# Kernel optimization log

Hardware: AMD Instinct MI355X
Metric: run time of the kernel (lower is better)

## Reference

```python
import jax, jax.numpy as jnp
import numpy as np

B, D, K, L, C = 1024, 512, 255, 256, 80  # batch, feat, internal nodes, leaves, classes
DEPTH = 8  # complete binary tree: 2^8 = 256 leaves


def _build_res_path():
    # res_path[l, k] = 1 if internal node k is on leaf l's path and leaf goes left,
    # -1 if it goes right, 0 if node k not on the path (matches build_tree_squeeze).
    rp = np.zeros((L, K), dtype=np.int32)
    for leaf in range(L):
        node = 0
        for d in range(DEPTH):
            bit = (leaf >> (DEPTH - 1 - d)) & 1  # 0 -> left, 1 -> right
            rp[leaf, node] = 1 if bit == 0 else -1
            node = 2 * node + 1 + bit
    return jnp.asarray(rp)


def setup_inputs() -> dict:
    key = jax.random.key(0)
    k1, k2, k3, k4 = jax.random.split(key, 4)
    x = jax.random.normal(k1, (B, D), dtype=jnp.float32)
    node_embeddings = jax.random.normal(k2, (K, D), dtype=jnp.float32)
    leaf_W = jax.random.normal(k3, (L * C, D), dtype=jnp.float32) * (1.0 / np.sqrt(D))
    leaf_b = jax.random.normal(k4, (L * C,), dtype=jnp.float32) * 0.01
    res_path = _build_res_path()
    return {"x": x, "node_embeddings": node_embeddings, "leaf_W": leaf_W,
            "leaf_b": leaf_b, "res_path": res_path}


def reference(x, node_embeddings, leaf_W, leaf_b, res_path):
    # L2-normalize node embeddings, cosine-sim routing probabilities
    ne = node_embeddings / jnp.linalg.norm(node_embeddings, axis=-1, keepdims=True)
    node_sim = jax.nn.sigmoid(jnp.einsum('bc,kc->bk', x, ne))  # [B, K]
    # leaf decision logits: Linear(D, L*C) reshaped to [B, L, C]
    leaf_dec = (jnp.einsum('bc,oc->bo', x, leaf_W) + leaf_b).reshape(x.shape[0], L, C)
    left_mask = (res_path == 1)[None]    # [1, L, K]
    right_mask = (res_path == -1)[None]  # [1, L, K]
    ns = node_sim[:, None, :]            # [B, 1, K]
    prob_left = jnp.prod(jnp.where(left_mask, ns, 1.0), axis=-1)        # [B, L]
    prob_right = jnp.prod(jnp.where(right_mask, 1.0 - ns, 1.0), axis=-1)  # [B, L]
    probs = (prob_left * prob_right)[..., None] * leaf_dec  # [B, L, C]
    return probs.sum(axis=1), node_sim
```

## Files before the change

kernel.cpp:

```cpp
#include <hip/hip_runtime.h>
#include <stdint.h>

#define B_  1024
#define D_  512
#define K_  255
#define L_  256
#define C_  80

typedef __attribute__((ext_vector_type(8))) short bf16x8;
typedef __attribute__((ext_vector_type(4))) float f32x4;

#define GLD(gsrc, ldst) \
  __builtin_amdgcn_global_load_lds((const __attribute__((address_space(1))) void*)(gsrc), \
                                   (__attribute__((address_space(3))) void*)(ldst), 16, 0, 0)

__device__ __forceinline__ short cvt_bf16(float f) {
    unsigned u = __float_as_uint(f);
    u += 0x7FFFu + ((u >> 16) & 1u);
    return (short)(u >> 16);
}

typedef __attribute__((ext_vector_type(8))) short short8;

__global__ void convert_kernel(const float* __restrict__ w, const float* __restrict__ x,
                               short* __restrict__ wb, short* __restrict__ xb) {
    size_t i0 = (size_t)blockIdx.x * blockDim.x + threadIdx.x;
    size_t stride = (size_t)gridDim.x * blockDim.x;
    for (size_t v = i0; v < 1310720u; v += stride) {
        float4 a = ((const float4*)w)[v * 2];
        float4 b = ((const float4*)w)[v * 2 + 1];
        short8 o;
        o[0] = cvt_bf16(a.x); o[1] = cvt_bf16(a.y); o[2] = cvt_bf16(a.z); o[3] = cvt_bf16(a.w);
        o[4] = cvt_bf16(b.x); o[5] = cvt_bf16(b.y); o[6] = cvt_bf16(b.z); o[7] = cvt_bf16(b.w);
        ((short8*)wb)[v] = o;
    }
    for (size_t v = i0; v < 65536u; v += stride) {
        float4 a = ((const float4*)x)[v * 2];
        float4 b = ((const float4*)x)[v * 2 + 1];
        short8 o;
        o[0] = cvt_bf16(a.x); o[1] = cvt_bf16(a.y); o[2] = cvt_bf16(a.z); o[3] = cvt_bf16(a.w);
        o[4] = cvt_bf16(b.x); o[5] = cvt_bf16(b.y); o[6] = cvt_bf16(b.z); o[7] = cvt_bf16(b.w);
        ((short8*)xb)[v] = o;
    }
}

__global__ __launch_bounds__(256) void node_kernel(const float* __restrict__ x,
                                                   const float* __restrict__ ne,
                                                   float* __restrict__ out1,
                                                   float* __restrict__ p_ws) {
    __shared__ __align__(16) float xs[4 * D_];
    __shared__ float ss[4 * K_];
    const int t = threadIdx.x;
    const int b0 = blockIdx.x * 4;

    const float4* xg = (const float4*)(x + (size_t)b0 * D_);
    ((float4*)xs)[t]       = xg[t];
    ((float4*)xs)[t + 256] = xg[t + 256];
    __syncthreads();

    if (t < K_) {
        const float4* nr = (const float4*)(ne + (size_t)t * D_);
        float acc0 = 0.f, acc1 = 0.f, acc2 = 0.f, acc3 = 0.f, nrm = 0.f;
        #pragma unroll 4
        for (int d4 = 0; d4 < D_ / 4; ++d4) {
            float4 nv = nr[d4];
            nrm += nv.x * nv.x + nv.y * nv.y + nv.z * nv.z + nv.w * nv.w;
            float4 x0 = ((const float4*)xs)[d4];
            float4 x1 = ((const float4*)xs)[128 + d4];
            float4 x2 = ((const float4*)xs)[256 + d4];
            float4 x3 = ((const float4*)xs)[384 + d4];
            acc0 += nv.x * x0.x + nv.y * x0.y + nv.z * x0.z + nv.w * x0.w;
            acc1 += nv.x * x1.x + nv.y * x1.y + nv.z * x1.z + nv.w * x1.w;
            acc2 += nv.x * x2.x + nv.y * x2.y + nv.z * x2.z + nv.w * x2.w;
            acc3 += nv.x * x3.x + nv.y * x3.y + nv.z * x3.z + nv.w * x3.w;
        }
        float inv = rsqrtf(nrm);
        float a[4] = {acc0, acc1, acc2, acc3};
        #pragma unroll
        for (int b = 0; b < 4; ++b) {
            float sig = 1.f / (1.f + __expf(-a[b] * inv));
            ss[b * K_ + t] = sig;
            out1[(size_t)(b0 + b) * K_ + t] = sig;
        }
    }
    __syncthreads();

    #pragma unroll
    for (int b = 0; b < 4; ++b) {
        float prob = 1.f;
        int node = 0;
        #pragma unroll
        for (int d = 0; d < 8; ++d) {
            int bit = (t >> (7 - d)) & 1;
            float s = ss[b * K_ + node];
            prob *= bit ? (1.f - s) : s;
            node = 2 * node + 1 + bit;
        }
        p_ws[(size_t)(b0 + b) * L_ + t] = prob;
    }
}

__global__ __launch_bounds__(256, 2) void gemm_kernel(const short* __restrict__ xb,
                                                      const short* __restrict__ wb,
                                                      const float* __restrict__ p,
                                                      const float* __restrict__ lb,
                                                      float* __restrict__ partial) {
    __shared__ __align__(16) short Ald[1024 * 8];
    __shared__ __align__(16) short Bld[640 * 8];
    __shared__ float p_ld[128];
    __shared__ float b_ld[80];

    const int tid  = threadIdx.x;
    const int lane = tid & 63;
    const int wave = tid >> 6;
    const int q    = lane >> 4;
    const int r    = lane & 15;
    const int wrow = wave * 32;
    const int mt   = blockIdx.x & 7;
    const int lc   = blockIdx.x >> 3;

    f32x4 outacc[2][5];
    #pragma unroll
    for (int mf = 0; mf < 2; ++mf)
        #pragma unroll
        for (int nf = 0; nf < 5; ++nf)
            outacc[mf][nf] = (f32x4){0.f, 0.f, 0.f, 0.f};

    const bf16x8* Av = (const bf16x8*)Ald;
    const bf16x8* Bv = (const bf16x8*)Bld;

    for (int li = 0; li < 4; ++li) {
        const int l = lc * 4 + li;
        f32x4 dec[2][5];
        #pragma unroll
        for (int mf = 0; mf < 2; ++mf)
            #pragma unroll
            for (int nf = 0; nf < 5; ++nf)
                dec[mf][nf] = (f32x4){0.f, 0.f, 0.f, 0.f};

        for (int kb = 0; kb < 8; ++kb) {
            __syncthreads();
            #pragma unroll
            for (int j = 0; j < 4; ++j) {
                int ph = j * 256 + tid;
                int rr = ph >> 3;
                int g  = (ph & 7) ^ (rr & 7);
                const short* src = xb + ((size_t)(mt * 128 + rr) * D_ + kb * 64 + g * 8);
                GLD(src, Ald + ph * 8);
            }
            #pragma unroll
            for (int j = 0; j < 2; ++j) {
                int ph = j * 256 + tid;
                int cc = ph >> 3;
                int g  = (ph & 7) ^ (cc & 7);
                const short* src = wb + ((size_t)(l * C_ + cc) * D_ + kb * 64 + g * 8);
                GLD(src, Bld + ph * 8);
            }
            if (tid < 128) {
                int ph = 512 + tid;
                int cc = ph >> 3;
                int g  = (ph & 7) ^ (cc & 7);
                const short* src = wb + ((size_t)(l * C_ + cc) * D_ + kb * 64 + g * 8);
                GLD(src, Bld + ph * 8);
            }
            if (kb == 0) {
                if (tid < 128) p_ld[tid] = p[(size_t)(mt * 128 + tid) * L_ + l];
                if (tid < 80)  b_ld[tid] = lb[l * C_ + tid];
            }
            __syncthreads();

            #pragma unroll
            for (int ks = 0; ks < 2; ++ks) {
                const int g = ks * 4 + q;
                bf16x8 af[2], bfr[5];
                #pragma unroll
                for (int mf = 0; mf < 2; ++mf) {
                    int rl = wrow + mf * 16 + r;
                    af[mf] = Av[rl * 8 + (g ^ (rl & 7))];
                }
                #pragma unroll
                for (int nf = 0; nf < 5; ++nf) {
                    int cl = nf * 16 + r;
                    bfr[nf] = Bv[cl * 8 + (g ^ (cl & 7))];
                }
                #pragma unroll
                for (int mf = 0; mf < 2; ++mf)
                    #pragma unroll
                    for (int nf = 0; nf < 5; ++nf)
                        dec[mf][nf] = __builtin_amdgcn_mfma_f32_16x16x32_bf16(
                            af[mf], bfr[nf], dec[mf][nf], 0, 0, 0);
            }
        }

        #pragma unroll
        for (int mf = 0; mf < 2; ++mf) {
            #pragma unroll
            for (int nf = 0; nf < 5; ++nf) {
                float bv = b_ld[nf * 16 + r];
                #pragma unroll
                for (int i = 0; i < 4; ++i) {
                    int row = wrow + mf * 16 + q * 4 + i;
                    outacc[mf][nf][i] += p_ld[row] * (dec[mf][nf][i] + bv);
                }
            }
        }
    }

    const size_t rbase = (size_t)lc * B_ + mt * 128;
    #pragma unroll
    for (int mf = 0; mf < 2; ++mf)
        #pragma unroll
        for (int nf = 0; nf < 5; ++nf)
            #pragma unroll
            for (int i = 0; i < 4; ++i) {
                int row = wrow + mf * 16 + q * 4 + i;
                int col = nf * 16 + r;
                partial[(rbase + row) * C_ + col] = outacc[mf][nf][i];
            }
}

__global__ void reduce_kernel(const float* __restrict__ partial, float* __restrict__ out0) {
    int idx = blockIdx.x * 256 + threadIdx.x;
    float s = 0.f;
    #pragma unroll 8
    for (int j = 0; j < 64; ++j)
        s += partial[(size_t)j * (B_ * C_) + idx];
    out0[idx] = s;
}

extern "C" void kernel_launch(void* const* d_in, const int* in_sizes, int n_in,
                              void* d_out, int out_size, void* d_ws, size_t ws_size,
                              hipStream_t stream) {
    const float* x  = (const float*)d_in[0];
    const float* ne = (const float*)d_in[1];
    const float* lW = (const float*)d_in[2];
    const float* lb = (const float*)d_in[3];

    float* out0 = (float*)d_out;
    float* out1 = out0 + (size_t)B_ * C_;

    char* ws = (char*)d_ws;
    float* p_ws    = (float*)ws;
    short* xb      = (short*)(ws + (1u << 20));
    short* wb      = (short*)(ws + (2u << 20));
    float* partial = (float*)(ws + (22u << 20));

    convert_kernel<<<2048, 256, 0, stream>>>(lW, x, wb, xb);
    node_kernel<<<B_ / 4, 256, 0, stream>>>(x, ne, out1, p_ws);
    gemm_kernel<<<512, 256, 0, stream>>>(xb, wb, p_ws, lb, partial);
    reduce_kernel<<<(B_ * C_) / 256, 256, 0, stream>>>(partial, out0);
}
```

Before: 154.8 us.

## Move node similarity to bf16 MFMA GEMM and restructure leaf GEMM tiling

Node embeddings are L2-normalized and converted to bf16 inside the convert kernel. The node-similarity dot products then run as a small MFMA GEMM in place of the scalar FP32 loop, and leaf probabilities are computed in a separate small kernel. The main leaf GEMM now gives each block two leaves (160 columns) over the full K with no outer leaf loop, uses 1024 blocks with a higher occupancy hint, and writes 128 partial slices, so the reduce kernel sums twice as many partials. This trades more partial-sum traffic and an extra launch for better MFMA use and parallelism, and node_sim now carries bf16 precision error.

New measurement: 143.1 us. -7.5%, faster.

```diff
diff --git a/kernel.cpp b/kernel.cpp
--- a/kernel.cpp
+++ b/kernel.cpp
@@ -9,6 +9,7 @@
 
 typedef __attribute__((ext_vector_type(8))) short bf16x8;
 typedef __attribute__((ext_vector_type(4))) float f32x4;
+typedef __attribute__((ext_vector_type(8))) short short8;
 
 #define GLD(gsrc, ldst) \
   __builtin_amdgcn_global_load_lds((const __attribute__((address_space(1))) void*)(gsrc), \
@@ -20,210 +21,227 @@
     return (short)(u >> 16);
 }
 
-typedef __attribute__((ext_vector_type(8))) short short8;
-
-__global__ void convert_kernel(const float* __restrict__ w, const float* __restrict__ x,
-                               short* __restrict__ wb, short* __restrict__ xb) {
-    size_t i0 = (size_t)blockIdx.x * blockDim.x + threadIdx.x;
-    size_t stride = (size_t)gridDim.x * blockDim.x;
-    for (size_t v = i0; v < 1310720u; v += stride) {
-        float4 a = ((const float4*)w)[v * 2];
-        float4 b = ((const float4*)w)[v * 2 + 1];
-        short8 o;
-        o[0] = cvt_bf16(a.x); o[1] = cvt_bf16(a.y); o[2] = cvt_bf16(a.z); o[3] = cvt_bf16(a.w);
-        o[4] = cvt_bf16(b.x); o[5] = cvt_bf16(b.y); o[6] = cvt_bf16(b.z); o[7] = cvt_bf16(b.w);
-        ((short8*)wb)[v] = o;
-    }
-    for (size_t v = i0; v < 65536u; v += stride) {
-        float4 a = ((const float4*)x)[v * 2];
-        float4 b = ((const float4*)x)[v * 2 + 1];
-        short8 o;
-        o[0] = cvt_bf16(a.x); o[1] = cvt_bf16(a.y); o[2] = cvt_bf16(a.z); o[3] = cvt_bf16(a.w);
-        o[4] = cvt_bf16(b.x); o[5] = cvt_bf16(b.y); o[6] = cvt_bf16(b.z); o[7] = cvt_bf16(b.w);
-        ((short8*)xb)[v] = o;
-    }
-}
-
-__global__ __launch_bounds__(256) void node_kernel(const float* __restrict__ x,
-                                                   const float* __restrict__ ne,
-                                                   float* __restrict__ out1,
-                                                   float* __restrict__ p_ws) {
-    __shared__ __align__(16) float xs[4 * D_];
-    __shared__ float ss[4 * K_];
-    const int t = threadIdx.x;
-    const int b0 = blockIdx.x * 4;
-
-    const float4* xg = (const float4*)(x + (size_t)b0 * D_);
-    ((float4*)xs)[t]       = xg[t];
-    ((float4*)xs)[t + 256] = xg[t + 256];
+__global__ __launch_bounds__(256) void convert_kernel(const float* __restrict__ w,
+                                                      const float* __restrict__ x,
+                                                      const float* __restrict__ ne,
+                                                      short* __restrict__ wb,
+                                                      short* __restrict__ xb,
+                                                      short* __restrict__ neb) {
+    __shared__ float red[256];
+    const int tid = threadIdx.x;
+    if (blockIdx.x < 2048) {
+        size_t i0 = (size_t)blockIdx.x * 256 + tid;
+        const size_t stride = 2048u * 256u;
+        for (size_t v = i0; v < 1310720u; v += stride) {
+            float4 a = ((const float4*)w)[v * 2];
+            float4 b = ((const float4*)w)[v * 2 + 1];
+            short8 o;
+            o[0] = cvt_bf16(a.x); o[1] = cvt_bf16(a.y); o[2] = cvt_bf16(a.z); o[3] = cvt_bf16(a.w);
+            o[4] = cvt_bf16(b.x); o[5] = cvt_bf16(b.y); o[6] = cvt_bf16(b.z); o[7] = cvt_bf16(b.w);
+            ((short8*)wb)[v] = o;
+        }
+        for (size_t v = i0; v < 65536u; v += stride) {
+            float4 a = ((const float4*)x)[v * 2];
+            float4 b = ((const float4*)x)[v * 2 + 1];
+            short8 o;
+            o[0] = cvt_bf16(a.x); o[1] = cvt_bf16(a.y); o[2] = cvt_bf16(a.z); o[3] = cvt_bf16(a.w);
+            o[4] = cvt_bf16(b.x); o[5] = cvt_bf16(b.y); o[6] = cvt_bf16(b.z); o[7] = cvt_bf16(b.w);
+            ((short8*)xb)[v] = o;
+        }
+    } else {
+        const int row = blockIdx.x - 2048;
+        if (row == 255) {
+            ((unsigned*)(neb + 255 * 512))[tid] = 0u;
+            return;
+        }
+        const float2* nr = (const float2*)(ne + (size_t)row * 512);
+        float2 a = nr[tid];
+        red[tid] = a.x * a.x + a.y * a.y;
+        __syncthreads();
+        #pragma unroll
+        for (int s = 128; s > 0; s >>= 1) {
+            if (tid < s) red[tid] += red[tid + s];
+            __syncthreads();
+        }
+        float inv = rsqrtf(red[0]);
+        unsigned lo = (unsigned short)cvt_bf16(a.x * inv);
+        unsigned hi = (unsigned short)cvt_bf16(a.y * inv);
+        ((unsigned*)(neb + (size_t)row * 512))[tid] = lo | (hi << 16);
+    }
+}
+
+__global__ __launch_bounds__(256) void simgemm_kernel(const short* __restrict__ xb,
+                                                      const short* __restrict__ neb,
+                                                      float* __restrict__ out1) {
+    __shared__ __align__(16) short Ald[512 * 8];
+    __shared__ __align__(16) short Bld[512 * 8];
+    const int tid = threadIdx.x;
+    const int lane = tid & 63, wave = tid >> 6;
+    const int q = lane >> 4, r = lane & 15;
+    const int mt = blockIdx.x >> 2;
+    const int nt = blockIdx.x & 3;
+
+    f32x4 acc[4];
+    #pragma unroll
+    for (int nf = 0; nf < 4; ++nf) acc[nf] = (f32x4){0.f, 0.f, 0.f, 0.f};
+
+    const bf16x8* Av = (const bf16x8*)Ald;
+    const bf16x8* Bv = (const bf16x8*)Bld;
+
+    for (int kb = 0; kb < 8; ++kb) {
+        __syncthreads();
+        #pragma unroll
+        for (int j = 0; j < 2; ++j) {
+            int ph = j * 256 + tid, rr = ph >> 3, g = (ph & 7) ^ (rr & 7);
+            GLD(xb + ((size_t)(mt * 64 + rr) * D_ + kb * 64 + g * 8), Ald + ph * 8);
+        }
+        #pragma unroll
+        for (int j = 0; j < 2; ++j) {
+            int ph = j * 256 + tid, cc = ph >> 3, g = (ph & 7) ^ (cc & 7);
+            GLD(neb + ((size_t)(nt * 64 + cc) * D_ + kb * 64 + g * 8), Bld + ph * 8);
+        }
+        __syncthreads();
+        #pragma unroll
+        for (int ks = 0; ks < 2; ++ks) {
+            const int g = ks * 4 + q;
+            int rl = wave * 16 + r;
+            bf16x8 af = Av[rl * 8 + (g ^ (rl & 7))];
+            #pragma unroll
+            for (int nf = 0; nf < 4; ++nf) {
+                int cl = nf * 16 + r;
+                bf16x8 bfr = Bv[cl * 8 + (g ^ (cl & 7))];
+                acc[nf] = __builtin_amdgcn_mfma_f32_16x16x32_bf16(af, bfr, acc[nf], 0, 0, 0);
+            }
+        }
+    }
+    #pragma unroll
+    for (int nf = 0; nf < 4; ++nf) {
+        int gcol = nt * 64 + nf * 16 + r;
+        if (gcol < K_) {
+            #pragma unroll
+            for (int i = 0; i < 4; ++i) {
+                int grow = mt * 64 + wave * 16 + q * 4 + i;
+                out1[(size_t)grow * K_ + gcol] = 1.f / (1.f + __expf(-acc[nf][i]));
+            }
+        }
+    }
+}
+
+__global__ __launch_bounds__(256) void leafprob_kernel(const float* __restrict__ out1,
+                                                       float* __restrict__ p_ws) {
+    __shared__ float ss[K_];
+    const int b = blockIdx.x, t = threadIdx.x;
+    if (t < K_) ss[t] = out1[(size_t)b * K_ + t];
     __syncthreads();
-
-    if (t < K_) {
-        const float4* nr = (const float4*)(ne + (size_t)t * D_);
-        float acc0 = 0.f, acc1 = 0.f, acc2 = 0.f, acc3 = 0.f, nrm = 0.f;
-        #pragma unroll 4
-        for (int d4 = 0; d4 < D_ / 4; ++d4) {
-            float4 nv = nr[d4];
-            nrm += nv.x * nv.x + nv.y * nv.y + nv.z * nv.z + nv.w * nv.w;
-            float4 x0 = ((const float4*)xs)[d4];
-            float4 x1 = ((const float4*)xs)[128 + d4];
-            float4 x2 = ((const float4*)xs)[256 + d4];
-            float4 x3 = ((const float4*)xs)[384 + d4];
-            acc0 += nv.x * x0.x + nv.y * x0.y + nv.z * x0.z + nv.w * x0.w;
-            acc1 += nv.x * x1.x + nv.y * x1.y + nv.z * x1.z + nv.w * x1.w;
-            acc2 += nv.x * x2.x + nv.y * x2.y + nv.z * x2.z + nv.w * x2.w;
-            acc3 += nv.x * x3.x + nv.y * x3.y + nv.z * x3.z + nv.w * x3.w;
-        }
-        float inv = rsqrtf(nrm);
-        float a[4] = {acc0, acc1, acc2, acc3};
-        #pragma unroll
-        for (int b = 0; b < 4; ++b) {
-            float sig = 1.f / (1.f + __expf(-a[b] * inv));
-            ss[b * K_ + t] = sig;
-            out1[(size_t)(b0 + b) * K_ + t] = sig;
-        }
-    }
-    __syncthreads();
-
-    #pragma unroll
-    for (int b = 0; b < 4; ++b) {
-        float prob = 1.f;
-        int node = 0;
-        #pragma unroll
-        for (int d = 0; d < 8; ++d) {
-            int bit = (t >> (7 - d)) & 1;
-            float s = ss[b * K_ + node];
-            prob *= bit ? (1.f - s) : s;
-            node = 2 * node + 1 + bit;
-        }
-        p_ws[(size_t)(b0 + b) * L_ + t] = prob;
-    }
-}
-
-__global__ __launch_bounds__(256, 2) void gemm_kernel(const short* __restrict__ xb,
+    float prob = 1.f;
+    int node = 0;
+    #pragma unroll
+    for (int d = 0; d < 8; ++d) {
+        int bit = (t >> (7 - d)) & 1;
+        float s = ss[node];
+        prob *= bit ? (1.f - s) : s;
+        node = 2 * node + 1 + bit;
+    }
+    p_ws[(size_t)b * L_ + t] = prob;
+}
+
+__global__ __launch_bounds__(256, 4) void gemm_kernel(const short* __restrict__ xb,
                                                       const short* __restrict__ wb,
                                                       const float* __restrict__ p,
                                                       const float* __restrict__ lb,
                                                       float* __restrict__ partial) {
     __shared__ __align__(16) short Ald[1024 * 8];
-    __shared__ __align__(16) short Bld[640 * 8];
-    __shared__ float p_ld[128];
-    __shared__ float b_ld[80];
-
-    const int tid  = threadIdx.x;
-    const int lane = tid & 63;
-    const int wave = tid >> 6;
-    const int q    = lane >> 4;
-    const int r    = lane & 15;
+    __shared__ __align__(16) short Bld[1280 * 8];
+    __shared__ float p_ld[128][2];
+    __shared__ float b_ld[160];
+
+    const int tid = threadIdx.x;
+    const int lane = tid & 63, wave = tid >> 6;
+    const int q = lane >> 4, r = lane & 15;
     const int wrow = wave * 32;
-    const int mt   = blockIdx.x & 7;
-    const int lc   = blockIdx.x >> 3;
-
-    f32x4 outacc[2][5];
+    const int lp = blockIdx.x & 127;
+    const int mt = blockIdx.x >> 7;
+
+    if (tid < 128) {
+        p_ld[tid][0] = p[(size_t)(mt * 128 + tid) * L_ + 2 * lp];
+        p_ld[tid][1] = p[(size_t)(mt * 128 + tid) * L_ + 2 * lp + 1];
+    }
+    if (tid < 160) b_ld[tid] = lb[lp * 160 + tid];
+
+    f32x4 dec[2][10];
     #pragma unroll
     for (int mf = 0; mf < 2; ++mf)
         #pragma unroll
-        for (int nf = 0; nf < 5; ++nf)
-            outacc[mf][nf] = (f32x4){0.f, 0.f, 0.f, 0.f};
+        for (int nf = 0; nf < 10; ++nf)
+            dec[mf][nf] = (f32x4){0.f, 0.f, 0.f, 0.f};
 
     const bf16x8* Av = (const bf16x8*)Ald;
     const bf16x8* Bv = (const bf16x8*)Bld;
 
-    for (int li = 0; li < 4; ++li) {
-        const int l = lc * 4 + li;
-        f32x4 dec[2][5];
-        #pragma unroll
-        for (int mf = 0; mf < 2; ++mf)
-            #pragma unroll
-            for (int nf = 0; nf < 5; ++nf)
-                dec[mf][nf] = (f32x4){0.f, 0.f, 0.f, 0.f};
-
-        for (int kb = 0; kb < 8; ++kb) {
-            __syncthreads();
-            #pragma unroll
-            for (int j = 0; j < 4; ++j) {
-                int ph = j * 256 + tid;
-                int rr = ph >> 3;
-                int g  = (ph & 7) ^ (rr & 7);
-                const short* src = xb + ((size_t)(mt * 128 + rr) * D_ + kb * 64 + g * 8);
-                GLD(src, Ald + ph * 8);
-            }
-            #pragma unroll
-            for (int j = 0; j < 2; ++j) {
-                int ph = j * 256 + tid;
-                int cc = ph >> 3;
-                int g  = (ph & 7) ^ (cc & 7);
-                const short* src = wb + ((size_t)(l * C_ + cc) * D_ + kb * 64 + g * 8);
-                GLD(src, Bld + ph * 8);
-            }
-            if (tid < 128) {
-                int ph = 512 + tid;
-                int cc = ph >> 3;
-                int g  = (ph & 7) ^ (cc & 7);
-                const short* src = wb + ((size_t)(l * C_ + cc) * D_ + kb * 64 + g * 8);
-                GLD(src, Bld + ph * 8);
-            }
-            if (kb == 0) {
-                if (tid < 128) p_ld[tid] = p[(size_t)(mt * 128 + tid) * L_ + l];
-                if (tid < 80)  b_ld[tid] = lb[l * C_ + tid];
-            }
-            __syncthreads();
-
-            #pragma unroll
-            for (int ks = 0; ks < 2; ++ks) {
-                const int g = ks * 4 + q;
-                bf16x8 af[2], bfr[5];
-                #pragma unroll
-                for (int mf = 0; mf < 2; ++mf) {
-                    int rl = wrow + mf * 16 + r;
-                    af[mf] = Av[rl * 8 + (g ^ (rl & 7))];
-                }
+    for (int kb = 0; kb < 8; ++kb) {
+        __syncthreads();
+        #pragma unroll
+        for (int j = 0; j < 4; ++j) {
+            int ph = j * 256 + tid, rr = ph >> 3, g = (ph & 7) ^ (rr & 7);
+            GLD(xb + ((size_t)(mt * 128 + rr) * D_ + kb * 64 + g * 8), Ald + ph * 8);
+        }
+        #pragma unroll
+        for (int j = 0; j < 5; ++j) {
+            int ph = j * 256 + tid, cc = ph >> 3, g = (ph & 7) ^ (cc & 7);
+            GLD(wb + ((size_t)(lp * 160 + cc) * D_ + kb * 64 + g * 8), Bld + ph * 8);
+        }
+        __syncthreads();
+        #pragma unroll
+        for (int ks = 0; ks < 2; ++ks) {
+            const int g = ks * 4 + q;
+            bf16x8 af[2];
+            #pragma unroll
+            for (int mf = 0; mf < 2; ++mf) {
+                int rl = wrow + mf * 16 + r;
+                af[mf] = Av[rl * 8 + (g ^ (rl & 7))];
+            }
+            #pragma unroll
+            for (int half = 0; half < 2; ++half) {
+                bf16x8 bfr[5];
                 #pragma unroll
                 for (int nf = 0; nf < 5; ++nf) {
-                    int cl = nf * 16 + r;
+                    int cl = half * 80 + nf * 16 + r;
                     bfr[nf] = Bv[cl * 8 + (g ^ (cl & 7))];
                 }
                 #pragma unroll
                 for (int mf = 0; mf < 2; ++mf)
                     #pragma unroll
                     for (int nf = 0; nf < 5; ++nf)
-                        dec[mf][nf] = __builtin_amdgcn_mfma_f32_16x16x32_bf16(
-                            af[mf], bfr[nf], dec[mf][nf], 0, 0, 0);
-            }
-        }
-
-        #pragma unroll
-        for (int mf = 0; mf < 2; ++mf) {
-            #pragma unroll
-            for (int nf = 0; nf < 5; ++nf) {
-                float bv = b_ld[nf * 16 + r];
-                #pragma unroll
-                for (int i = 0; i < 4; ++i) {
-                    int row = wrow + mf * 16 + q * 4 + i;
-                    outacc[mf][nf][i] += p_ld[row] * (dec[mf][nf][i] + bv);
-                }
-            }
-        }
-    }
-
-    const size_t rbase = (size_t)lc * B_ + mt * 128;
-    #pragma unroll
-    for (int mf = 0; mf < 2; ++mf)
-        #pragma unroll
-        for (int nf = 0; nf < 5; ++nf)
+                        dec[mf][half * 5 + nf] = __builtin_amdgcn_mfma_f32_16x16x32_bf16(
+                            af[mf], bfr[nf], dec[mf][half * 5 + nf], 0, 0, 0);
+            }
+        }
+    }
+
+    const size_t rbase = (size_t)lp * B_ + mt * 128;
+    #pragma unroll
+    for (int mf = 0; mf < 2; ++mf) {
+        #pragma unroll
+        for (int nf = 0; nf < 5; ++nf) {
+            int c = nf * 16 + r;
+            float b0 = b_ld[c], b1 = b_ld[80 + c];
             #pragma unroll
             for (int i = 0; i < 4; ++i) {
                 int row = wrow + mf * 16 + q * 4 + i;
-                int col = nf * 16 + r;
-                partial[(rbase + row) * C_ + col] = outacc[mf][nf][i];
-            }
-}
-
-__global__ void reduce_kernel(const float* __restrict__ partial, float* __restrict__ out0) {
+                float v = p_ld[row][0] * (dec[mf][nf][i] + b0)
+                        + p_ld[row][1] * (dec[mf][nf + 5][i] + b1);
+                partial[(rbase + row) * C_ + c] = v;
+            }
+        }
+    }
+}
+
+__global__ __launch_bounds__(256) void reduce_kernel(const float* __restrict__ partial,
+                                                     float* __restrict__ out0) {
     int idx = blockIdx.x * 256 + threadIdx.x;
     float s = 0.f;
     #pragma unroll 8
-    for (int j = 0; j < 64; ++j)
+    for (int j = 0; j < 128; ++j)
         s += partial[(size_t)j * (B_ * C_) + idx];
     out0[idx] = s;
 }
@@ -240,13 +258,15 @@
     float* out1 = out0 + (size_t)B_ * C_;
 
     char* ws = (char*)d_ws;
-    float* p_ws    = (float*)ws;
-    short* xb      = (short*)(ws + (1u << 20));
-    short* wb      = (short*)(ws + (2u << 20));
-    float* partial = (float*)(ws + (22u << 20));
-
-    convert_kernel<<<2048, 256, 0, stream>>>(lW, x, wb, xb);
-    node_kernel<<<B_ / 4, 256, 0, stream>>>(x, ne, out1, p_ws);
-    gemm_kernel<<<512, 256, 0, stream>>>(xb, wb, p_ws, lb, partial);
+    short* xb      = (short*)ws;
+    short* neb     = (short*)(ws + (1u << 20));
+    float* p_ws    = (float*)(ws + (1u << 20) + (1u << 18));
+    short* wb      = (short*)(ws + (9u << 18));
+    float* partial = (float*)(ws + (24u << 20));
+
+    convert_kernel<<<2304, 256, 0, stream>>>(lW, x, ne, wb, xb, neb);
+    simgemm_kernel<<<64, 256, 0, stream>>>(xb, neb, out1);
+    leafprob_kernel<<<B_, 256, 0, stream>>>(out1, p_ws);
+    gemm_kernel<<<1024, 256, 0, stream>>>(xb, wb, p_ws, lb, partial);
     reduce_kernel<<<(B_ * C_) / 256, 256, 0, stream>>>(partial, out0);
 }
```
